# Kernel tuning notes

Measured on AMD Instinct MI355X. Metric: run time of the kernel, lower is better.

## Reference

```python
import jax, jax.numpy as jnp
import numpy as np


def setup_inputs() -> dict:
    key = jax.random.key(0)
    kq, kk, kv = jax.random.split(key, 3)
    B, Q, K, D = 8, 2048, 2048, 1024
    return {
        "queries": jax.random.normal(kq, (B, Q, D), dtype=jnp.float32),
        "keys": jax.random.normal(kk, (B, K, D), dtype=jnp.float32),
        "values": jax.random.normal(kv, (B, K, D), dtype=jnp.float32),
    }


def reference(queries, keys, values):
    # scores: [B, Q, K] = queries @ keys^T
    scores = jnp.einsum("bqd,bkd->bqk", queries, keys)
    # NOTE: softmax over dim=1, i.e. the QUERY axis (non-standard)
    attn = jax.nn.softmax(scores, axis=1)
    # output: [B, Q, D]
    return jnp.einsum("bqk,bkd->bqd", attn, values)
```

## Files before the change

### kernel.cpp

```cpp
#include <hip/hip_runtime.h>
#include <stdint.h>

typedef _Float16 half8 __attribute__((ext_vector_type(8)));
typedef __attribute__((ext_vector_type(4))) float f32x4;
typedef __attribute__((ext_vector_type(4))) unsigned short us4;
typedef __attribute__((ext_vector_type(8))) unsigned short us8;

#define BM 128
#define BN 128
#define BKK 32

__device__ inline unsigned short f2h(float x) {
  _Float16 h = (_Float16)x;
  return __builtin_bit_cast(unsigned short, h);
}

__device__ inline void ld16(const unsigned short* g, unsigned short* l) {
  __builtin_amdgcn_global_load_lds(
      (const __attribute__((address_space(1))) unsigned int*)g,
      (__attribute__((address_space(3))) unsigned int*)l, 16, 0, 0);
}

__global__ void k_cast16(const float* __restrict__ in, unsigned short* __restrict__ o, long n8) {
  long i = (long)blockIdx.x * blockDim.x + threadIdx.x;
  if (i >= n8) return;
  float4 a = ((const float4*)in)[i * 2];
  float4 b = ((const float4*)in)[i * 2 + 1];
  us8 h;
  h[0] = f2h(a.x); h[1] = f2h(a.y); h[2] = f2h(a.z); h[3] = f2h(a.w);
  h[4] = f2h(b.x); h[5] = f2h(b.y); h[6] = f2h(b.z); h[7] = f2h(b.w);
  *(us8*)(o + i * 8) = h;
}

__global__ void k_transpose16(const float* __restrict__ V, unsigned short* __restrict__ VT,
                              int Kn, int Dn) {
  __shared__ unsigned short t[64][65];
  const int b = blockIdx.z;
  const int k0 = blockIdx.x * 64, d0 = blockIdx.y * 64;
  const int c = threadIdx.x & 63, rr = threadIdx.x >> 6;
  const float* pV = V + (long)b * Kn * Dn;
  unsigned short* pT = VT + (long)b * Dn * Kn;
#pragma unroll
  for (int i = 0; i < 16; ++i) {
    int r = rr + i * 4;
    t[r][c] = f2h(pV[(long)(k0 + r) * Dn + d0 + c]);
  }
  __syncthreads();
#pragma unroll
  for (int i = 0; i < 16; ++i) {
    int r = rr + i * 4;
    pT[(long)(d0 + r) * Kn + k0 + c] = t[c][r];
  }
}

template <int STATS>
__launch_bounds__(256)
__global__ void k_gemm_bt(const unsigned short* __restrict__ A,
                          const unsigned short* __restrict__ B,
                          float* __restrict__ C, float2* __restrict__ ps,
                          int N, int Kin, long sA, long sB, long sC) {
  __shared__ unsigned short sA_[BM * BKK];
  __shared__ unsigned short sB_[BN * BKK];

  const int b = blockIdx.z;
  const int tm = blockIdx.y, tn = blockIdx.x;
  const int tid = threadIdx.x;
  const int lane = tid & 63;
  const int wave = tid >> 6;
  const int wm = (wave & 1) * 64, wn = (wave >> 1) * 64;

  const unsigned short* pA = A + b * sA + (long)tm * BM * Kin;
  const unsigned short* pB = B + b * sB + (long)tn * BN * Kin;
  float* pC = C + b * sC;

  const int c0 = tid, c1 = tid + 256;
  const long ga0 = (long)(c0 >> 2) * Kin + (c0 & 3) * 8;
  const long ga1 = (long)(c1 >> 2) * Kin + (c1 & 3) * 8;

  f32x4 acc[4][4];
#pragma unroll
  for (int i = 0; i < 4; ++i)
#pragma unroll
    for (int j = 0; j < 4; ++j)
#pragma unroll
      for (int r = 0; r < 4; ++r) acc[i][j][r] = 0.f;

  const int mrow = wm + (lane & 15);
  const int nrow = wn + (lane & 15);
  const int kq = (lane >> 4) * 8;

  const int nk = Kin / BKK;
  for (int kt = 0; kt < nk; ++kt) {
    const long kb = (long)kt * BKK;
    __syncthreads();
    ld16(pA + ga0 + kb, &sA_[c0 * 8]);
    ld16(pA + ga1 + kb, &sA_[c1 * 8]);
    ld16(pB + ga0 + kb, &sB_[c0 * 8]);
    ld16(pB + ga1 + kb, &sB_[c1 * 8]);
    __syncthreads();

    half8 af[4], bf[4];
#pragma unroll
    for (int i = 0; i < 4; ++i) {
      af[i] = *(const half8*)&sA_[(mrow + i * 16) * BKK + kq];
      bf[i] = *(const half8*)&sB_[(nrow + i * 16) * BKK + kq];
    }
#pragma unroll
    for (int i = 0; i < 4; ++i)
#pragma unroll
      for (int j = 0; j < 4; ++j)
        acc[i][j] = __builtin_amdgcn_mfma_f32_16x16x32_f16(af[i], bf[j], acc[i][j], 0, 0, 0);
  }

  const int crow0 = tm * BM + wm + (lane >> 4) * 4;
  const int ccol0 = tn * BN + wn + (lane & 15);
#pragma unroll
  for (int i = 0; i < 4; ++i)
#pragma unroll
    for (int j = 0; j < 4; ++j)
#pragma unroll
      for (int r = 0; r < 4; ++r)
        pC[(long)(crow0 + i * 16 + r) * N + (ccol0 + j * 16)] = acc[i][j][r];

  if constexpr (STATS) {
#pragma unroll
    for (int j = 0; j < 4; ++j) {
      float m = -3.0e38f;
#pragma unroll
      for (int i = 0; i < 4; ++i)
#pragma unroll
        for (int r = 0; r < 4; ++r) m = fmaxf(m, acc[i][j][r]);
      m = fmaxf(m, __shfl_xor(m, 16, 64));
      m = fmaxf(m, __shfl_xor(m, 32, 64));
      float l = 0.f;
#pragma unroll
      for (int i = 0; i < 4; ++i)
#pragma unroll
        for (int r = 0; r < 4; ++r) l += __expf(acc[i][j][r] - m);
      l += __shfl_xor(l, 16, 64);
      l += __shfl_xor(l, 32, 64);
      if (lane < 16) {
        int col = tn * BN + wn + j * 16 + lane;
        ps[((long)(b * 32 + tm * 2 + (wave & 1))) * N + col] = make_float2(m, l);
      }
    }
  }
}

__global__ void k_stats_combine(const float2* __restrict__ ps, float2* __restrict__ st, int Kn) {
  const long i = (long)blockIdx.x * blockDim.x + threadIdx.x;
  const int b = (int)(i / Kn), k = (int)(i % Kn);
  float M = -3.0e38f;
#pragma unroll
  for (int j = 0; j < 32; ++j) M = fmaxf(M, ps[((long)(b * 32 + j)) * Kn + k].x);
  float L = 0.f;
#pragma unroll
  for (int j = 0; j < 32; ++j) {
    float2 v = ps[((long)(b * 32 + j)) * Kn + k];
    L += v.y * __expf(v.x - M);
  }
  st[i] = make_float2(M, 1.0f / L);
}

__global__ void k_pcomp(const float* __restrict__ S, const float2* __restrict__ st,
                        unsigned short* __restrict__ P) {
  const long i = (long)blockIdx.x * blockDim.x + threadIdx.x;
  const long r = i >> 8;
  const int kb = (int)(i & 255) * 8;
  const int b = (int)(r >> 11);
  const float* sp = S + r * 2048 + kb;
  float4 s0 = *(const float4*)sp;
  float4 s1 = *(const float4*)(sp + 4);
  const float2* tp = st + (long)b * 2048 + kb;
  us8 o;
  float sv[8] = {s0.x, s0.y, s0.z, s0.w, s1.x, s1.y, s1.z, s1.w};
#pragma unroll
  for (int j = 0; j < 8; ++j) {
    float2 t = tp[j];
    o[j] = f2h(__expf(sv[j] - t.x) * t.y);
  }
  *(us8*)(P + r * 2048 + kb) = o;
}

extern "C" void kernel_launch(void* const* d_in, const int* in_sizes, int n_in,
                              void* d_out, int out_size, void* d_ws, size_t ws_size,
                              hipStream_t stream) {
  const float* Q = (const float*)d_in[0];
  const float* Kp = (const float*)d_in[1];
  const float* V = (const float*)d_in[2];
  float* out = (float*)d_out;

  constexpr int Bb = 8, Qn = 2048, Kn = 2048, Dn = 1024;
  constexpr long QD = (long)Qn * Dn, KD = (long)Kn * Dn, QK = (long)Qn * Kn, DK = (long)Dn * Kn;

  const size_t per = 3 * (size_t)(QD * 2)
                   + (size_t)(QK * 4)
                   + (size_t)(QK * 2)
                   + (size_t)(32 * Kn * 8)
                   + (size_t)(Kn * 8);
  int cb = 8;
  while (cb > 1 && (size_t)cb * per > ws_size) cb >>= 1;

  char* w = (char*)d_ws;
  unsigned short* q16 = (unsigned short*)w; w += (size_t)cb * QD * 2;
  unsigned short* k16 = (unsigned short*)w; w += (size_t)cb * KD * 2;
  unsigned short* vt  = (unsigned short*)w; w += (size_t)cb * DK * 2;
  float* S            = (float*)w;          w += (size_t)cb * QK * 4;
  unsigned short* P   = (unsigned short*)w; w += (size_t)cb * QK * 2;
  float2* ps          = (float2*)w;         w += (size_t)cb * 32 * Kn * 8;
  float2* st          = (float2*)w;

  for (int b0 = 0; b0 < Bb; b0 += cb) {
    int nb = (cb < Bb - b0) ? cb : (Bb - b0);
    long n8 = (long)nb * QD / 8;
    k_cast16<<<(int)(n8 / 256), 256, 0, stream>>>(Q + b0 * QD, q16, n8);
    k_cast16<<<(int)(n8 / 256), 256, 0, stream>>>(Kp + b0 * KD, k16, n8);
    k_transpose16<<<dim3(Kn / 64, Dn / 64, nb), 256, 0, stream>>>(V + b0 * KD, vt, Kn, Dn);
    k_gemm_bt<1><<<dim3(Kn / 128, Qn / 128, nb), 256, 0, stream>>>(
        q16, k16, S, ps, Kn, Dn, QD, KD, QK);
    k_stats_combine<<<nb * Kn / 256, 256, 0, stream>>>(ps, st, Kn);
    k_pcomp<<<(int)((long)nb * QK / 8 / 256), 256, 0, stream>>>(S, st, P);
    k_gemm_bt<0><<<dim3(Dn / 128, Qn / 128, nb), 256, 0, stream>>>(
        P, vt, out + b0 * QD, nullptr, Dn, Kn, QK, DK, QD);
  }
}
```

Measured before the change: 498.4 us.

## Rewrite GEMM as 256x256 tile, 8-wave, 4-stage LDS pipeline with swizzle

The fp16 MFMA GEMM moves from 128x128 tiles with 4 waves and a single LDS buffer to 256x256 tiles with 8 waves, a 4-slot LDS ring fed by direct global-to-LDS loads, and explicit waitcnt and barrier phasing with MFMA priority raised. LDS layout is XOR-swizzled to cut bank conflicts, and workgroup IDs are remapped across XCDs for cache locality. The goal is to hide global load latency and raise MFMA utilization and data reuse. The stats partials shrink from 32 to 16 row-tiles per batch to match. In exchange it uses much more LDS and registers (8x4 accumulators per wave), launches fewer blocks, and depends on hand-tuned waitcnt counts being correct.

```diff
diff --git a/kernel.cpp b/kernel.cpp
--- a/kernel.cpp
+++ b/kernel.cpp
@@ -3,12 +3,7 @@
 
 typedef _Float16 half8 __attribute__((ext_vector_type(8)));
 typedef __attribute__((ext_vector_type(4))) float f32x4;
-typedef __attribute__((ext_vector_type(4))) unsigned short us4;
 typedef __attribute__((ext_vector_type(8))) unsigned short us8;
-
-#define BM 128
-#define BN 128
-#define BKK 32
 
 __device__ inline unsigned short f2h(float x) {
   _Float16 h = (_Float16)x;
@@ -53,95 +48,168 @@
   }
 }
 
+
+#define SBAR() __builtin_amdgcn_s_barrier()
+#define SCHED0() __builtin_amdgcn_sched_barrier(0)
+#define LGKM0() do { asm volatile("s_waitcnt lgkmcnt(0)" ::: "memory"); SCHED0(); } while (0)
+#define VMC(n) do { asm volatile("s_waitcnt vmcnt(" #n ")" ::: "memory"); } while (0)
+
 template <int STATS>
-__launch_bounds__(256)
+__launch_bounds__(512, 2)
 __global__ void k_gemm_bt(const unsigned short* __restrict__ A,
                           const unsigned short* __restrict__ B,
                           float* __restrict__ C, float2* __restrict__ ps,
                           int N, int Kin, long sA, long sB, long sC) {
-  __shared__ unsigned short sA_[BM * BKK];
-  __shared__ unsigned short sB_[BN * BKK];
-
-  const int b = blockIdx.z;
-  const int tm = blockIdx.y, tn = blockIdx.x;
+  __shared__ unsigned short sAb[4][256 * 32];
+  __shared__ unsigned short sBb[4][256 * 32];
+
   const int tid = threadIdx.x;
-  const int lane = tid & 63;
-  const int wave = tid >> 6;
-  const int wm = (wave & 1) * 64, wn = (wave >> 1) * 64;
-
-  const unsigned short* pA = A + b * sA + (long)tm * BM * Kin;
-  const unsigned short* pB = B + b * sB + (long)tn * BN * Kin;
+  const int lane = tid & 63, wave = tid >> 6;
+  const int wr = wave >> 2, wc = wave & 3;
+  const int l15 = lane & 15;
+
+  const int nx = gridDim.x, ny = gridDim.y;
+  int wg = ((int)blockIdx.z * ny + blockIdx.y) * nx + blockIdx.x;
+  const int nwg = nx * ny * (int)gridDim.z;
+  wg = (wg & 7) * (nwg >> 3) + (wg >> 3);
+  const int tn = wg % nx, tm = (wg / nx) % ny, b = wg / (nx * ny);
+
+  const unsigned short* pA = A + b * sA + (long)tm * 256 * Kin;
+  const unsigned short* pB = B + b * sB + (long)tn * 256 * Kin;
   float* pC = C + b * sC;
 
-  const int c0 = tid, c1 = tid + 256;
-  const long ga0 = (long)(c0 >> 2) * Kin + (c0 & 3) * 8;
-  const long ga1 = (long)(c1 >> 2) * Kin + (c1 & 3) * 8;
-
-  f32x4 acc[4][4];
-#pragma unroll
-  for (int i = 0; i < 4; ++i)
+  const int rlo = tid >> 2;
+  const int csw = ((tid & 3) * 8) ^ (((rlo >> 1) & 3) << 3);
+  const long ga = (long)rlo * Kin + csw;
+  const long gh = (long)128 * Kin;
+
+  const int ksw = ((lane >> 4) * 8) ^ (((l15 >> 1) & 3) << 3);
+  const int aoff = (wr * 128 + l15) * 32 + ksw;
+  const int boff = (wc * 64 + l15) * 32 + ksw;
+
+#define STG_A(t, q) do { \
+    ld16(pA + ga + (long)(t) * 32, &sAb[q][tid * 8]); \
+    ld16(pA + ga + gh + (long)(t) * 32, &sAb[q][4096 + tid * 8]); } while (0)
+#define STG_B(t, q) do { \
+    ld16(pB + ga + (long)(t) * 32, &sBb[q][tid * 8]); \
+    ld16(pB + ga + gh + (long)(t) * 32, &sBb[q][4096 + tid * 8]); } while (0)
+
+#define LDA8(q, m) (*(const half8*)&sAb[q][aoff + (m) * 512])
+#define LDB8(q, n) (*(const half8*)&sBb[q][boff + (n) * 512])
+
+  f32x4 acc[8][4];
+#pragma unroll
+  for (int i = 0; i < 8; ++i)
 #pragma unroll
     for (int j = 0; j < 4; ++j)
 #pragma unroll
       for (int r = 0; r < 4; ++r) acc[i][j][r] = 0.f;
 
-  const int mrow = wm + (lane & 15);
-  const int nrow = wn + (lane & 15);
-  const int kq = (lane >> 4) * 8;
-
-  const int nk = Kin / BKK;
-  for (int kt = 0; kt < nk; ++kt) {
-    const long kb = (long)kt * BKK;
-    __syncthreads();
-    ld16(pA + ga0 + kb, &sA_[c0 * 8]);
-    ld16(pA + ga1 + kb, &sA_[c1 * 8]);
-    ld16(pB + ga0 + kb, &sB_[c0 * 8]);
-    ld16(pB + ga1 + kb, &sB_[c1 * 8]);
-    __syncthreads();
-
-    half8 af[4], bf[4];
-#pragma unroll
-    for (int i = 0; i < 4; ++i) {
-      af[i] = *(const half8*)&sA_[(mrow + i * 16) * BKK + kq];
-      bf[i] = *(const half8*)&sB_[(nrow + i * 16) * BKK + kq];
-    }
-#pragma unroll
-    for (int i = 0; i < 4; ++i)
-#pragma unroll
-      for (int j = 0; j < 4; ++j)
-        acc[i][j] = __builtin_amdgcn_mfma_f32_16x16x32_f16(af[i], bf[j], acc[i][j], 0, 0, 0);
-  }
-
-  const int crow0 = tm * BM + wm + (lane >> 4) * 4;
-  const int ccol0 = tn * BN + wn + (lane & 15);
-#pragma unroll
-  for (int i = 0; i < 4; ++i)
-#pragma unroll
-    for (int j = 0; j < 4; ++j)
+  half8 fa0, fa1, fa2, fa3, fb0, fb1, fb2, fb3;
+
+#define MFMA4(m, a) \
+  acc[m][0] = __builtin_amdgcn_mfma_f32_16x16x32_f16(a, fb0, acc[m][0], 0, 0, 0); \
+  acc[m][1] = __builtin_amdgcn_mfma_f32_16x16x32_f16(a, fb1, acc[m][1], 0, 0, 0); \
+  acc[m][2] = __builtin_amdgcn_mfma_f32_16x16x32_f16(a, fb2, acc[m][2], 0, 0, 0); \
+  acc[m][3] = __builtin_amdgcn_mfma_f32_16x16x32_f16(a, fb3, acc[m][3], 0, 0, 0);
+
+#define PH_READ_AB(q) \
+  fa0 = LDA8(q, 0); fa1 = LDA8(q, 1); fa2 = LDA8(q, 2); fa3 = LDA8(q, 3); \
+  fb0 = LDB8(q, 0); fb1 = LDB8(q, 1); fb2 = LDB8(q, 2); fb3 = LDB8(q, 3);
+
+#define PH_READ_A(q) \
+  fa0 = LDA8(q, 4); fa1 = LDA8(q, 5); fa2 = LDA8(q, 6); fa3 = LDA8(q, 7);
+
+#define PH_MFMA_LO \
+  __builtin_amdgcn_s_setprio(1); \
+  MFMA4(0, fa0) MFMA4(1, fa1) MFMA4(2, fa2) MFMA4(3, fa3) \
+  __builtin_amdgcn_s_setprio(0);
+
+#define PH_MFMA_HI \
+  __builtin_amdgcn_s_setprio(1); \
+  MFMA4(4, fa0) MFMA4(5, fa1) MFMA4(6, fa2) MFMA4(7, fa3) \
+  __builtin_amdgcn_s_setprio(0);
+
+  const int nt = Kin >> 5;
+  const int ni = nt >> 1;
+
+  STG_A(0, 0); STG_B(0, 0);
+  STG_A(1, 1); STG_B(1, 1);
+  VMC(4); SCHED0(); SBAR();
+
+  for (int it = 0; it + 1 < ni; ++it) {
+    const int t0 = it * 2;
+    const int q0 = t0 & 3, q1 = q0 + 1;
+    const int r0 = q0 ^ 2, r1 = q1 ^ 2;
+    PH_READ_AB(q0)
+    STG_A(t0 + 2, r0);
+    SCHED0(); SBAR(); LGKM0();
+    PH_MFMA_LO
+    SCHED0(); SBAR();
+    PH_READ_A(q0)
+    STG_B(t0 + 2, r0);
+    SCHED0(); SBAR(); LGKM0();
+    PH_MFMA_HI
+    VMC(4); SCHED0(); SBAR();
+    PH_READ_AB(q1)
+    STG_A(t0 + 3, r1);
+    SCHED0(); SBAR(); LGKM0();
+    PH_MFMA_LO
+    SCHED0(); SBAR();
+    PH_READ_A(q1)
+    STG_B(t0 + 3, r1);
+    SCHED0(); SBAR(); LGKM0();
+    PH_MFMA_HI
+    VMC(4); SCHED0(); SBAR();
+  }
+  {
+    const int q0 = (nt - 2) & 3, q1 = q0 + 1;
+    PH_READ_AB(q0)
+    SCHED0(); SBAR(); LGKM0();
+    PH_MFMA_LO
+    SCHED0(); SBAR();
+    PH_READ_A(q0)
+    SCHED0(); SBAR(); LGKM0();
+    PH_MFMA_HI
+    VMC(0); SCHED0(); SBAR();
+    PH_READ_AB(q1)
+    LGKM0();
+    PH_MFMA_LO
+    PH_READ_A(q1)
+    LGKM0();
+    PH_MFMA_HI
+  }
+
+  const int crow0 = tm * 256 + wr * 128 + (lane >> 4) * 4;
+  const int ccol0 = tn * 256 + wc * 64 + l15;
+#pragma unroll
+  for (int m = 0; m < 8; ++m)
+#pragma unroll
+    for (int n = 0; n < 4; ++n)
 #pragma unroll
       for (int r = 0; r < 4; ++r)
-        pC[(long)(crow0 + i * 16 + r) * N + (ccol0 + j * 16)] = acc[i][j][r];
+        pC[(long)(crow0 + m * 16 + r) * N + ccol0 + n * 16] = acc[m][n][r];
 
   if constexpr (STATS) {
 #pragma unroll
-    for (int j = 0; j < 4; ++j) {
-      float m = -3.0e38f;
-#pragma unroll
-      for (int i = 0; i < 4; ++i)
-#pragma unroll
-        for (int r = 0; r < 4; ++r) m = fmaxf(m, acc[i][j][r]);
-      m = fmaxf(m, __shfl_xor(m, 16, 64));
-      m = fmaxf(m, __shfl_xor(m, 32, 64));
+    for (int n = 0; n < 4; ++n) {
+      float mx = -3.0e38f;
+#pragma unroll
+      for (int m = 0; m < 8; ++m)
+#pragma unroll
+        for (int r = 0; r < 4; ++r) mx = fmaxf(mx, acc[m][n][r]);
+      mx = fmaxf(mx, __shfl_xor(mx, 16, 64));
+      mx = fmaxf(mx, __shfl_xor(mx, 32, 64));
       float l = 0.f;
 #pragma unroll
-      for (int i = 0; i < 4; ++i)
-#pragma unroll
-        for (int r = 0; r < 4; ++r) l += __expf(acc[i][j][r] - m);
+      for (int m = 0; m < 8; ++m)
+#pragma unroll
+        for (int r = 0; r < 4; ++r) l += __expf(acc[m][n][r] - mx);
       l += __shfl_xor(l, 16, 64);
       l += __shfl_xor(l, 32, 64);
       if (lane < 16) {
-        int col = tn * BN + wn + j * 16 + lane;
-        ps[((long)(b * 32 + tm * 2 + (wave & 1))) * N + col] = make_float2(m, l);
+        int col = tn * 256 + wc * 64 + n * 16 + lane;
+        ps[((long)(b * 16 + tm * 2 + wr)) * N + col] = make_float2(mx, l);
       }
     }
   }
@@ -152,11 +220,11 @@
   const int b = (int)(i / Kn), k = (int)(i % Kn);
   float M = -3.0e38f;
 #pragma unroll
-  for (int j = 0; j < 32; ++j) M = fmaxf(M, ps[((long)(b * 32 + j)) * Kn + k].x);
+  for (int j = 0; j < 16; ++j) M = fmaxf(M, ps[((long)(b * 16 + j)) * Kn + k].x);
   float L = 0.f;
 #pragma unroll
-  for (int j = 0; j < 32; ++j) {
-    float2 v = ps[((long)(b * 32 + j)) * Kn + k];
+  for (int j = 0; j < 16; ++j) {
+    float2 v = ps[((long)(b * 16 + j)) * Kn + k];
     L += v.y * __expf(v.x - M);
   }
   st[i] = make_float2(M, 1.0f / L);
@@ -196,7 +264,7 @@
   const size_t per = 3 * (size_t)(QD * 2)
                    + (size_t)(QK * 4)
                    + (size_t)(QK * 2)
-                   + (size_t)(32 * Kn * 8)
+                   + (size_t)(16 * Kn * 8)
                    + (size_t)(Kn * 8);
   int cb = 8;
   while (cb > 1 && (size_t)cb * per > ws_size) cb >>= 1;
@@ -207,7 +275,7 @@
   unsigned short* vt  = (unsigned short*)w; w += (size_t)cb * DK * 2;
   float* S            = (float*)w;          w += (size_t)cb * QK * 4;
   unsigned short* P   = (unsigned short*)w; w += (size_t)cb * QK * 2;
-  float2* ps          = (float2*)w;         w += (size_t)cb * 32 * Kn * 8;
+  float2* ps          = (float2*)w;         w += (size_t)cb * 16 * Kn * 8;
   float2* st          = (float2*)w;
 
   for (int b0 = 0; b0 < Bb; b0 += cb) {
@@ -216,11 +284,11 @@
     k_cast16<<<(int)(n8 / 256), 256, 0, stream>>>(Q + b0 * QD, q16, n8);
     k_cast16<<<(int)(n8 / 256), 256, 0, stream>>>(Kp + b0 * KD, k16, n8);
     k_transpose16<<<dim3(Kn / 64, Dn / 64, nb), 256, 0, stream>>>(V + b0 * KD, vt, Kn, Dn);
-    k_gemm_bt<1><<<dim3(Kn / 128, Qn / 128, nb), 256, 0, stream>>>(
+    k_gemm_bt<1><<<dim3(Kn / 256, Qn / 256, nb), 512, 0, stream>>>(
         q16, k16, S, ps, Kn, Dn, QD, KD, QK);
     k_stats_combine<<<nb * Kn / 256, 256, 0, stream>>>(ps, st, Kn);
     k_pcomp<<<(int)((long)nb * QK / 8 / 256), 256, 0, stream>>>(S, st, P);
-    k_gemm_bt<0><<<dim3(Dn / 128, Qn / 128, nb), 256, 0, stream>>>(
+    k_gemm_bt<0><<<dim3(Dn / 256, Qn / 256, nb), 512, 0, stream>>>(
         P, vt, out + b0 * QD, nullptr, Dn, Kn, QK, DK, QD);
   }
 }
```

New measurement: 460.0 us. 1.08x faster.
